# Kernel tuning notes

Hardware: AMD Instinct MI355X
Metric: run time of the kernel (lower is better)

The kernel has to match this reference:

```python
import jax, jax.numpy as jnp
import numpy as np

N_NODES = 50000
N_EDGES = 800000
IN_CH, OUT_CH, HEADS = 64, 32, 4
NEG_SLOPE = 0.2
BN_EPS = 1e-5


def setup_inputs() -> dict:
    key = jax.random.key(0)
    ks = jax.random.split(key, 9)
    x = jax.random.normal(ks[0], (N_NODES, IN_CH), dtype=jnp.float32)
    pos = jax.random.uniform(ks[1], (N_NODES, 3), dtype=jnp.float32)
    edge_index = jax.random.randint(ks[2], (2, N_EDGES), 0, N_NODES, dtype=jnp.int64)
    s = 1.0 / np.sqrt(IN_CH)
    W_l = jax.random.normal(ks[3], (IN_CH, HEADS * OUT_CH), dtype=jnp.float32) * s
    W_r = jax.random.normal(ks[4], (IN_CH, HEADS * OUT_CH), dtype=jnp.float32) * s
    W_edge = jax.random.normal(ks[5], (3, HEADS * OUT_CH), dtype=jnp.float32) * 0.5
    att = jax.random.normal(ks[6], (HEADS, OUT_CH), dtype=jnp.float32) * (1.0 / np.sqrt(OUT_CH))
    bn_gamma = jax.random.uniform(ks[7], (HEADS * OUT_CH,), dtype=jnp.float32, minval=0.5, maxval=1.5)
    bn_beta = jax.random.normal(ks[8], (HEADS * OUT_CH,), dtype=jnp.float32) * 0.1
    return {"x": x, "pos": pos, "edge_index": edge_index, "W_l": W_l, "W_r": W_r,
            "W_edge": W_edge, "att": att, "bn_gamma": bn_gamma, "bn_beta": bn_beta}


def reference(x, pos, edge_index, W_l, W_r, W_edge, att, bn_gamma, bn_beta):
    N = x.shape[0]
    H, C = att.shape
    # source->target projections (GATv2: lin_l for source/messages, lin_r for target)
    xl = (x @ W_l).reshape(N, H, C)
    xr = (x @ W_r).reshape(N, H, C)
    src, dst = edge_index[0], edge_index[1]
    edge_attr = pos[src] - pos[dst]  # [E,3] relative position as edge feature
    # add self-loops with fill_value='mean' (PyG default)
    loop = jnp.arange(N)
    src = jnp.concatenate([src, loop])
    dst = jnp.concatenate([dst, loop])
    mean_attr = edge_attr.mean(axis=0, keepdims=True)  # [1,3]
    edge_attr = jnp.concatenate([edge_attr, jnp.broadcast_to(mean_attr, (N, 3))], axis=0)
    # per-edge GATv2 score: att . LeakyReLU(x_l[j] + x_r[i] + W_e e_ij)
    e_feat = (edge_attr @ W_edge).reshape(-1, H, C)
    msg = xl[src]                              # [Et,H,C] (reused for aggregation)
    e = msg + xr[dst] + e_feat
    e = jax.nn.leaky_relu(e, NEG_SLOPE)
    score = jnp.einsum('ehc,hc->eh', e, att)   # [Et,H]
    # segment softmax over destination node
    m = jax.ops.segment_max(score, dst, num_segments=N)
    score = jnp.exp(score - m[dst])
    denom = jax.ops.segment_sum(score, dst, num_segments=N)
    alpha = score / (denom[dst] + 1e-16)       # [Et,H]
    out = jax.ops.segment_sum(alpha[:, :, None] * msg, dst, num_segments=N)
    out = out.reshape(N, H * C)
    # BatchNorm over node dimension (training-mode batch statistics, PyG BatchNorm)
    mu = out.mean(axis=0)
    var = out.var(axis=0)
    return (out - mu) / jnp.sqrt(var + BN_EPS) * bn_gamma + bn_beta
```

## Files before the change

### kernel.cpp

```cpp
#include <hip/hip_runtime.h>
#include <hip/hip_bf16.h>
#include <hip/hip_fp16.h>

#define N_NODES 50000
#define IN_CH 64
#define HC 128
#define CAP 64
#define NEG_SLOPE 0.2f
#define BN_EPS 1e-5f


__global__ __launch_bounds__(256) void k_gemm(const float* __restrict__ x,
                                              const float* __restrict__ Wl,
                                              const float* __restrict__ Wr,
                                              unsigned int* __restrict__ xl_bf,
                                              float* __restrict__ xr_out,
                                              int* __restrict__ deg,
                                              float* __restrict__ mean_sums,
                                              float* __restrict__ bn_sums,
                                              int* __restrict__ flag,
                                              const int* __restrict__ eidx) {
  {
    int gtid = blockIdx.x * 256 + threadIdx.x;
    if (gtid < N_NODES) deg[gtid] = 1;
    if (gtid < 256) bn_sums[gtid] = 0.f;
    if (gtid < 3) mean_sums[gtid] = 0.f;
    if (blockIdx.x == 0 && threadIdx.x < 64) {
      int w = eidx[2 * threadIdx.x + 1];
      unsigned long long nz = __ballot(w != 0);
      if (threadIdx.x == 0) flag[0] = (nz == 0ULL) ? 1 : 0;
    }
  }

  __shared__ float xs[16][IN_CH];
  __shared__ __hip_bfloat162 wsm[IN_CH][128];
  const int t = threadIdx.x;
  const int row0 = blockIdx.x * 16;

  for (int i = 0; i < 32; ++i) {
    int k = i * 2 + (t >> 7);
    int p = t & 127;
    int cc = p * 2;
    float2 wv;
    if (cc < 128) wv = *(const float2*)(Wl + k * 128 + cc);
    else          wv = *(const float2*)(Wr + k * 128 + (cc - 128));
    wsm[k][p] = __float22bfloat162_rn(wv);
  }
  {
    int r = t >> 4, c4 = (t & 15) * 4;
    *(float4*)&xs[r][c4] = *(const float4*)(x + (row0 + r) * IN_CH + c4);
  }
  __syncthreads();

  const int ct = t & 63;
  const int rt = t >> 6;
  const int c4 = ct * 4;
  const int r4 = rt * 4;

  float acc[4][4];
  #pragma unroll
  for (int a = 0; a < 4; ++a)
    #pragma unroll
    for (int b = 0; b < 4; ++b) acc[a][b] = 0.f;

  #pragma unroll 8
  for (int k = 0; k < IN_CH; ++k) {
    uint2 wraw = *(const uint2*)&wsm[k][ct * 2];
    float2 f01 = __bfloat1622float2(*(__hip_bfloat162*)&wraw.x);
    float2 f23 = __bfloat1622float2(*(__hip_bfloat162*)&wraw.y);
    float wv[4] = {f01.x, f01.y, f23.x, f23.y};
    float xv[4] = {xs[r4][k], xs[r4 + 1][k], xs[r4 + 2][k], xs[r4 + 3][k]};
    #pragma unroll
    for (int a = 0; a < 4; ++a)
      #pragma unroll
      for (int b = 0; b < 4; ++b) acc[a][b] = fmaf(xv[a], wv[b], acc[a][b]);
  }

  #pragma unroll
  for (int a = 0; a < 4; ++a) {
    int row = row0 + r4 + a;
    if (c4 < 128) {
      __hip_bfloat162 b01 = __float22bfloat162_rn(make_float2(acc[a][0], acc[a][1]));
      __hip_bfloat162 b23 = __float22bfloat162_rn(make_float2(acc[a][2], acc[a][3]));
      uint2 u;
      u.x = *(unsigned int*)&b01;
      u.y = *(unsigned int*)&b23;
      *(uint2*)(xl_bf + row * 64 + (c4 >> 1)) = u;
    } else {
      float4 v = make_float4(acc[a][0], acc[a][1], acc[a][2], acc[a][3]);
      *(float4*)(xr_out + row * HC + (c4 - 128)) = v;
    }
  }
}

__device__ __forceinline__ uint2 packslot(int s, float dx, float dy, float dz) {
  __half2 hxy = __halves2half2(__float2half_rn(dx), __float2half_rn(dy));
  uint2 r;
  r.x = *(unsigned int*)&hxy;
  r.y = ((unsigned int)s << 16) | (unsigned int)__half_as_ushort(__float2half_rn(dz));
  return r;
}

__global__ __launch_bounds__(256) void k_edges(const int* __restrict__ eidx,
                                               const float* __restrict__ pos,
                                               int* __restrict__ deg,
                                               uint2* __restrict__ bucket,
                                               float* __restrict__ mean_sums,
                                               const int* __restrict__ flag,
                                               int E) {
  const bool w64 = flag[0] != 0;
  const int tid = blockIdx.x * 256 + threadIdx.x;
  const int base = tid * 8;
  float sx = 0.f, sy = 0.f, sz = 0.f;

  const bool vec_ok = w64 ? ((E & 1) == 0) : ((E & 3) == 0);

  if (base + 8 <= E && vec_ok) {
    int s[8], d[8];
    if (w64) {
      const int4* ps = (const int4*)(eidx + 2 * base);
      int4 A = ps[0], B = ps[1], C = ps[2], D = ps[3];
      s[0]=A.x; s[1]=A.z; s[2]=B.x; s[3]=B.z; s[4]=C.x; s[5]=C.z; s[6]=D.x; s[7]=D.z;
      const int4* pd = (const int4*)(eidx + 2 * E + 2 * base);
      A = pd[0]; B = pd[1]; C = pd[2]; D = pd[3];
      d[0]=A.x; d[1]=A.z; d[2]=B.x; d[3]=B.z; d[4]=C.x; d[5]=C.z; d[6]=D.x; d[7]=D.z;
    } else {
      int4 A = *(const int4*)(eidx + base);
      int4 B = *(const int4*)(eidx + base + 4);
      s[0]=A.x; s[1]=A.y; s[2]=A.z; s[3]=A.w; s[4]=B.x; s[5]=B.y; s[6]=B.z; s[7]=B.w;
      A = *(const int4*)(eidx + E + base);
      B = *(const int4*)(eidx + E + base + 4);
      d[0]=A.x; d[1]=A.y; d[2]=A.z; d[3]=A.w; d[4]=B.x; d[5]=B.y; d[6]=B.z; d[7]=B.w;
    }
    int slot[8];
    #pragma unroll
    for (int k = 0; k < 8; ++k) slot[k] = atomicAdd(&deg[d[k]], 1);
    float dx[8], dy[8], dz[8];
    #pragma unroll
    for (int k = 0; k < 8; ++k) {
      dx[k] = pos[3 * s[k]]     - pos[3 * d[k]];
      dy[k] = pos[3 * s[k] + 1] - pos[3 * d[k] + 1];
      dz[k] = pos[3 * s[k] + 2] - pos[3 * d[k] + 2];
      sx += dx[k]; sy += dy[k]; sz += dz[k];
    }
    #pragma unroll
    for (int k = 0; k < 8; ++k)
      if (slot[k] < CAP) bucket[d[k] * CAP + slot[k]] = packslot(s[k], dx[k], dy[k], dz[k]);
  } else if (base < E) {
    int hi = min(base + 8, E);
    for (int e = base; e < hi; ++e) {
      int s, d;
      if (w64) { s = eidx[2 * e]; d = eidx[2 * (E + e)]; }
      else     { s = eidx[e];     d = eidx[E + e]; }
      int o = atomicAdd(&deg[d], 1);
      float dx = pos[3 * s]     - pos[3 * d];
      float dy = pos[3 * s + 1] - pos[3 * d + 1];
      float dz = pos[3 * s + 2] - pos[3 * d + 2];
      sx += dx; sy += dy; sz += dz;
      if (o < CAP) bucket[d * CAP + o] = packslot(s, dx, dy, dz);
    }
  }

  #pragma unroll
  for (int m = 1; m < 64; m <<= 1) {
    sx += __shfl_xor(sx, m); sy += __shfl_xor(sy, m); sz += __shfl_xor(sz, m);
  }
  __shared__ float red[4][3];
  int wave = threadIdx.x >> 6, lane = threadIdx.x & 63;
  if (lane == 0) { red[wave][0] = sx; red[wave][1] = sy; red[wave][2] = sz; }
  __syncthreads();
  if (threadIdx.x == 0) {
    float a = 0.f, b = 0.f, c = 0.f;
    for (int w = 0; w < 4; ++w) { a += red[w][0]; b += red[w][1]; c += red[w][2]; }
    unsafeAtomicAdd(&mean_sums[0], a);
    unsafeAtomicAdd(&mean_sums[1], b);
    unsafeAtomicAdd(&mean_sums[2], c);
  }
}

__device__ __forceinline__ float sum8_dpp(float v) {
  v += __int_as_float(__builtin_amdgcn_mov_dpp(__float_as_int(v), 0xB1, 0xF, 0xF, true));
  v += __int_as_float(__builtin_amdgcn_mov_dpp(__float_as_int(v), 0x4E, 0xF, 0xF, true));
  v += __int_as_float(__builtin_amdgcn_mov_dpp(__float_as_int(v), 0x141, 0xF, 0xF, true));
  return v;
}

__device__ __forceinline__ void edge_compute(uint2 raw, float dx, float dy, float dz, bool valid,
                                             const float4& xr4, const float4& at4,
                                             const float4& w0, const float4& w1, const float4& w2,
                                             float& a0, float& a1, float& a2, float& a3, float& den) {
  float2 x01 = __bfloat1622float2(*(__hip_bfloat162*)&raw.x);
  float2 x23 = __bfloat1622float2(*(__hip_bfloat162*)&raw.y);
  float t0 = x01.x + xr4.x; t0 = fmaf(dx, w0.x, t0); t0 = fmaf(dy, w1.x, t0); t0 = fmaf(dz, w2.x, t0);
  float t1 = x01.y + xr4.y; t1 = fmaf(dx, w0.y, t1); t1 = fmaf(dy, w1.y, t1); t1 = fmaf(dz, w2.y, t1);
  float t2 = x23.x + xr4.z; t2 = fmaf(dx, w0.z, t2); t2 = fmaf(dy, w1.z, t2); t2 = fmaf(dz, w2.z, t2);
  float t3 = x23.y + xr4.w; t3 = fmaf(dx, w0.w, t3); t3 = fmaf(dy, w1.w, t3); t3 = fmaf(dz, w2.w, t3);
  float l0 = fmaxf(t0, NEG_SLOPE * t0);
  float l1 = fmaxf(t1, NEG_SLOPE * t1);
  float l2 = fmaxf(t2, NEG_SLOPE * t2);
  float l3 = fmaxf(t3, NEG_SLOPE * t3);
  float sc = l0 * at4.x;
  sc = fmaf(l1, at4.y, sc); sc = fmaf(l2, at4.z, sc); sc = fmaf(l3, at4.w, sc);
  sc = sum8_dpp(sc);
  float e = __expf(sc);
  float p = valid ? e : 0.f;
  den += p;
  a0 = fmaf(p, x01.x, a0); a1 = fmaf(p, x01.y, a1);
  a2 = fmaf(p, x23.x, a2); a3 = fmaf(p, x23.y, a3);
}

__device__ __forceinline__ void slotNZ(const uint2* __restrict__ row, int j, int di, int i,
                                       int& s, float& dx, float& dy, float& dz, bool& v) {
  uint2 w = row[j];
  v = j < di;
  s = v ? (int)(w.y >> 16) : i;
  float2 dd = __half22float2(*(__half2*)&w.x);
  dx = dd.x; dy = dd.y;
  dz = __half2float(__ushort_as_half((unsigned short)(w.y & 0xffffu)));
}

__global__ __launch_bounds__(256) void k_agg(const unsigned int* __restrict__ xl_bf,
                                             float* __restrict__ xr_out,
                                             const float* __restrict__ att,
                                             const float* __restrict__ We,
                                             const float* __restrict__ mean_sums,
                                             const uint2* __restrict__ bucket,
                                             const int* __restrict__ deg,
                                             float invE,
                                             float* __restrict__ bn_sums) {
  __shared__ uint2 rowbuf[4][2][72];
  __shared__ __align__(16) float redS[4][128];
  __shared__ __align__(16) float redQ[4][128];

  const int lane = threadIdx.x & 63;
  const int half = lane >> 5;
  const int l5 = lane & 31;
  const int c = l5 << 2;
  const int wave = threadIdx.x >> 6;

  const float4 at4 = *(const float4*)(att + c);
  const float4 w0 = *(const float4*)(We + c);
  const float4 w1 = *(const float4*)(We + 128 + c);
  const float4 w2 = *(const float4*)(We + 256 + c);
  const float m0 = mean_sums[0] * invE;
  const float m1 = mean_sums[1] * invE;
  const float m2 = mean_sums[2] * invE;

  const int gw = blockIdx.x * 4 + wave;
  const int W = gridDim.x * 4;

  float4 bs = make_float4(0.f, 0.f, 0.f, 0.f);
  float4 bq = make_float4(0.f, 0.f, 0.f, 0.f);

  int dcur = min(deg[gw], CAP);
  if (lane < dcur) rowbuf[wave][0][lane] = bucket[gw * CAP + lane];
  int r = 0;

  for (int i = gw; i < N_NODES; i += W) {
    const int inext = i + W;
    int dnext = 0;
    uint2 sregN = make_uint2(0u, 0u);
    if (inext < N_NODES) {
      dnext = min(deg[inext], CAP);
      if (lane < dnext) sregN = bucket[inext * CAP + lane];
    }

    const uint2* row = rowbuf[wave][r];
    const float4 xr4 = *(const float4*)(xr_out + i * HC + c);
    const int di = dcur;

    int sA, sB;
    float dxA, dyA, dzA, dxB, dyB, dzB;
    bool vA, vB;
    if (half == 0) { sA = i; dxA = m0; dyA = m1; dzA = m2; vA = true; }
    else           { slotNZ(row, 1, di, i, sA, dxA, dyA, dzA, vA); }
    slotNZ(row, 2 + half, di, i, sB, dxB, dyB, dzB, vB);
    uint2 rawA = *(const uint2*)(xl_bf + (sA << 6) + (l5 << 1));
    uint2 rawB = *(const uint2*)(xl_bf + (sB << 6) + (l5 << 1));

    float a0 = 0.f, a1 = 0.f, a2 = 0.f, a3 = 0.f, den = 0.f;

    for (int j = 4; j < di; j += 4) {
      int sAn, sBn;
      float dxAn, dyAn, dzAn, dxBn, dyBn, dzBn;
      bool vAn, vBn;
      slotNZ(row, j + half,     di, i, sAn, dxAn, dyAn, dzAn, vAn);
      slotNZ(row, j + 2 + half, di, i, sBn, dxBn, dyBn, dzBn, vBn);
      uint2 rawAn = *(const uint2*)(xl_bf + (sAn << 6) + (l5 << 1));
      uint2 rawBn = *(const uint2*)(xl_bf + (sBn << 6) + (l5 << 1));

      edge_compute(rawA, dxA, dyA, dzA, vA, xr4, at4, w0, w1, w2, a0, a1, a2, a3, den);
      edge_compute(rawB, dxB, dyB, dzB, vB, xr4, at4, w0, w1, w2, a0, a1, a2, a3, den);

      rawA = rawAn; dxA = dxAn; dyA = dyAn; dzA = dzAn; vA = vAn;
      rawB = rawBn; dxB = dxBn; dyB = dyBn; dzB = dzBn; vB = vBn;
    }
    edge_compute(rawA, dxA, dyA, dzA, vA, xr4, at4, w0, w1, w2, a0, a1, a2, a3, den);
    edge_compute(rawB, dxB, dyB, dzB, vB, xr4, at4, w0, w1, w2, a0, a1, a2, a3, den);

    if (lane < dnext) rowbuf[wave][r ^ 1][lane] = sregN;

    den += __shfl_xor(den, 32);
    a0 += __shfl_xor(a0, 32);
    a1 += __shfl_xor(a1, 32);
    a2 += __shfl_xor(a2, 32);
    a3 += __shfl_xor(a3, 32);

    const float inv = 1.f / (den + 1e-16f);
    if (half == 0) {
      float4 o = make_float4(a0 * inv, a1 * inv, a2 * inv, a3 * inv);
      *(float4*)(xr_out + i * HC + c) = o;
      bs.x += o.x; bs.y += o.y; bs.z += o.z; bs.w += o.w;
      bq.x = fmaf(o.x, o.x, bq.x); bq.y = fmaf(o.y, o.y, bq.y);
      bq.z = fmaf(o.z, o.z, bq.z); bq.w = fmaf(o.w, o.w, bq.w);
    }

    dcur = dnext; r ^= 1;
  }

  if (half == 0) {
    *(float4*)&redS[wave][c] = bs;
    *(float4*)&redQ[wave][c] = bq;
  }
  __syncthreads();
  const int t = threadIdx.x;
  if (t < 128) {
    float s = redS[0][t] + redS[1][t] + redS[2][t] + redS[3][t];
    float q = redQ[0][t] + redQ[1][t] + redQ[2][t] + redQ[3][t];
    unsafeAtomicAdd(&bn_sums[t], s);
    unsafeAtomicAdd(&bn_sums[128 + t], q);
  }
}

__global__ __launch_bounds__(256) void k_bnapply(float* __restrict__ out,
                                                 const float* __restrict__ bn_sums,
                                                 const float* __restrict__ gamma,
                                                 const float* __restrict__ beta,
                                                 int n4) {
  const int stride = gridDim.x * blockDim.x;
  const float invN = 1.f / (float)N_NODES;
  for (int i = blockIdx.x * blockDim.x + threadIdx.x; i < n4; i += stride) {
    int c = (i & 31) * 4;
    float4 v = ((float4*)out)[i];
    float4 s = *(const float4*)(bn_sums + c);
    float4 q = *(const float4*)(bn_sums + 128 + c);
    float4 g = *(const float4*)(gamma + c);
    float4 b = *(const float4*)(beta + c);
    float mu, var, rstd;
    mu = s.x * invN; var = q.x * invN - mu * mu; rstd = rsqrtf(var + BN_EPS);
    v.x = (v.x - mu) * rstd * g.x + b.x;
    mu = s.y * invN; var = q.y * invN - mu * mu; rstd = rsqrtf(var + BN_EPS);
    v.y = (v.y - mu) * rstd * g.y + b.y;
    mu = s.z * invN; var = q.z * invN - mu * mu; rstd = rsqrtf(var + BN_EPS);
    v.z = (v.z - mu) * rstd * g.z + b.z;
    mu = s.w * invN; var = q.w * invN - mu * mu; rstd = rsqrtf(var + BN_EPS);
    v.w = (v.w - mu) * rstd * g.w + b.w;
    ((float4*)out)[i] = v;
  }
}

extern "C" void kernel_launch(void* const* d_in, const int* in_sizes, int n_in,
                              void* d_out, int out_size, void* d_ws, size_t ws_size,
                              hipStream_t stream) {
  const float* x     = (const float*)d_in[0];
  const float* pos   = (const float*)d_in[1];
  const int*   eidx  = (const int*)d_in[2];
  const float* Wl    = (const float*)d_in[3];
  const float* Wr    = (const float*)d_in[4];
  const float* We    = (const float*)d_in[5];
  const float* att   = (const float*)d_in[6];
  const float* gamma = (const float*)d_in[7];
  const float* beta  = (const float*)d_in[8];
  float* out = (float*)d_out;
  const int E = in_sizes[2] / 2;

  char* ws = (char*)d_ws;
  int*   flag      = (int*)(ws + 0);
  float* mean_sums = (float*)(ws + 64);
  float* bn_sums   = (float*)(ws + 1024);
  int*   deg       = (int*)(ws + 4096);
  uint2* bucket    = (uint2*)(ws + (1 << 19));
  unsigned int* xl_bf = (unsigned int*)(ws + (1 << 19) + (size_t)N_NODES * CAP * 8);

  k_gemm<<<N_NODES / 16, 256, 0, stream>>>(x, Wl, Wr, xl_bf, out,
                                           deg, mean_sums, bn_sums, flag, eidx);
  int eblocks = (E + 2047) / 2048;
  k_edges<<<eblocks, 256, 0, stream>>>(eidx, pos, deg, bucket, mean_sums, flag, E);
  k_agg<<<2048, 256, 0, stream>>>(xl_bf, out, att, We, mean_sums, bucket, deg,
                                  1.f / (float)E, bn_sums);
  k_bnapply<<<512, 256, 0, stream>>>(out, bn_sums, gamma, beta, out_size / 4);
}
```

Baseline: 243.9 us.

## Process one edge per wave with 2 channels per lane and readlane metadata

The aggregation kernel changes its work split. Each wave now handles one edge at a time, with every lane owning two channels, instead of two half-waves each handling alternate edges with four channels per lane. Edge metadata now sits in registers and is broadcast with readlane, replacing the LDS row buffer. The next node's xr row and self-loop xl row are prefetched as well. This removes LDS traffic, the cross-half shuffles and the padded invalid-slot work, but it serializes edges within a wave and adds one more DPP reduction step per edge.

```diff
diff --git a/kernel.cpp b/kernel.cpp
--- a/kernel.cpp
+++ b/kernel.cpp
@@ -178,45 +178,32 @@
   }
 }
 
-__device__ __forceinline__ float sum8_dpp(float v) {
-  v += __int_as_float(__builtin_amdgcn_mov_dpp(__float_as_int(v), 0xB1, 0xF, 0xF, true));
-  v += __int_as_float(__builtin_amdgcn_mov_dpp(__float_as_int(v), 0x4E, 0xF, 0xF, true));
+__device__ __forceinline__ float sum16_dpp(float v) {
+  v += __int_as_float(__builtin_amdgcn_mov_dpp(__float_as_int(v), 0xB1,  0xF, 0xF, true));
+  v += __int_as_float(__builtin_amdgcn_mov_dpp(__float_as_int(v), 0x4E,  0xF, 0xF, true));
   v += __int_as_float(__builtin_amdgcn_mov_dpp(__float_as_int(v), 0x141, 0xF, 0xF, true));
+  v += __int_as_float(__builtin_amdgcn_mov_dpp(__float_as_int(v), 0x140, 0xF, 0xF, true));
   return v;
 }
 
-__device__ __forceinline__ void edge_compute(uint2 raw, float dx, float dy, float dz, bool valid,
-                                             const float4& xr4, const float4& at4,
-                                             const float4& w0, const float4& w1, const float4& w2,
-                                             float& a0, float& a1, float& a2, float& a3, float& den) {
-  float2 x01 = __bfloat1622float2(*(__hip_bfloat162*)&raw.x);
-  float2 x23 = __bfloat1622float2(*(__hip_bfloat162*)&raw.y);
-  float t0 = x01.x + xr4.x; t0 = fmaf(dx, w0.x, t0); t0 = fmaf(dy, w1.x, t0); t0 = fmaf(dz, w2.x, t0);
-  float t1 = x01.y + xr4.y; t1 = fmaf(dx, w0.y, t1); t1 = fmaf(dy, w1.y, t1); t1 = fmaf(dz, w2.y, t1);
-  float t2 = x23.x + xr4.z; t2 = fmaf(dx, w0.z, t2); t2 = fmaf(dy, w1.z, t2); t2 = fmaf(dz, w2.z, t2);
-  float t3 = x23.y + xr4.w; t3 = fmaf(dx, w0.w, t3); t3 = fmaf(dy, w1.w, t3); t3 = fmaf(dz, w2.w, t3);
+__device__ __forceinline__ void edge2(unsigned raw, float dx, float dy, float dz,
+                                      const float2& xr2, const float2& at2,
+                                      const float2& w0, const float2& w1, const float2& w2,
+                                      float& den, float& a0, float& a1) {
+  float x0 = __uint_as_float(raw << 16);
+  float x1 = __uint_as_float(raw & 0xffff0000u);
+  float t0 = x0 + xr2.x;
+  t0 = fmaf(dx, w0.x, t0); t0 = fmaf(dy, w1.x, t0); t0 = fmaf(dz, w2.x, t0);
+  float t1 = x1 + xr2.y;
+  t1 = fmaf(dx, w0.y, t1); t1 = fmaf(dy, w1.y, t1); t1 = fmaf(dz, w2.y, t1);
   float l0 = fmaxf(t0, NEG_SLOPE * t0);
   float l1 = fmaxf(t1, NEG_SLOPE * t1);
-  float l2 = fmaxf(t2, NEG_SLOPE * t2);
-  float l3 = fmaxf(t3, NEG_SLOPE * t3);
-  float sc = l0 * at4.x;
-  sc = fmaf(l1, at4.y, sc); sc = fmaf(l2, at4.z, sc); sc = fmaf(l3, at4.w, sc);
-  sc = sum8_dpp(sc);
-  float e = __expf(sc);
-  float p = valid ? e : 0.f;
+  float sc = l0 * at2.x;
+  sc = fmaf(l1, at2.y, sc);
+  sc = sum16_dpp(sc);
+  float p = __expf(sc);
   den += p;
-  a0 = fmaf(p, x01.x, a0); a1 = fmaf(p, x01.y, a1);
-  a2 = fmaf(p, x23.x, a2); a3 = fmaf(p, x23.y, a3);
-}
-
-__device__ __forceinline__ void slotNZ(const uint2* __restrict__ row, int j, int di, int i,
-                                       int& s, float& dx, float& dy, float& dz, bool& v) {
-  uint2 w = row[j];
-  v = j < di;
-  s = v ? (int)(w.y >> 16) : i;
-  float2 dd = __half22float2(*(__half2*)&w.x);
-  dx = dd.x; dy = dd.y;
-  dz = __half2float(__ushort_as_half((unsigned short)(w.y & 0xffffu)));
+  a0 = fmaf(p, x0, a0); a1 = fmaf(p, x1, a1);
 }
 
 __global__ __launch_bounds__(256) void k_agg(const unsigned int* __restrict__ xl_bf,
@@ -228,20 +215,17 @@
                                              const int* __restrict__ deg,
                                              float invE,
                                              float* __restrict__ bn_sums) {
-  __shared__ uint2 rowbuf[4][2][72];
   __shared__ __align__(16) float redS[4][128];
   __shared__ __align__(16) float redQ[4][128];
 
   const int lane = threadIdx.x & 63;
-  const int half = lane >> 5;
-  const int l5 = lane & 31;
-  const int c = l5 << 2;
   const int wave = threadIdx.x >> 6;
-
-  const float4 at4 = *(const float4*)(att + c);
-  const float4 w0 = *(const float4*)(We + c);
-  const float4 w1 = *(const float4*)(We + 128 + c);
-  const float4 w2 = *(const float4*)(We + 256 + c);
+  const int c2 = lane << 1;
+
+  const float2 at2 = *(const float2*)(att + c2);
+  const float2 w0 = *(const float2*)(We + c2);
+  const float2 w1 = *(const float2*)(We + 128 + c2);
+  const float2 w2 = *(const float2*)(We + 256 + c2);
   const float m0 = mean_sums[0] * invE;
   const float m1 = mean_sums[1] * invE;
   const float m2 = mean_sums[2] * invE;
@@ -249,79 +233,72 @@
   const int gw = blockIdx.x * 4 + wave;
   const int W = gridDim.x * 4;
 
-  float4 bs = make_float4(0.f, 0.f, 0.f, 0.f);
-  float4 bq = make_float4(0.f, 0.f, 0.f, 0.f);
-
-  int dcur = min(deg[gw], CAP);
-  if (lane < dcur) rowbuf[wave][0][lane] = bucket[gw * CAP + lane];
-  int r = 0;
+  float bsx = 0.f, bsy = 0.f, bqx = 0.f, bqy = 0.f;
+
+  int dcur = 0;
+  uint2 rowc = make_uint2(0u, 0u);
+  float2 xrc = make_float2(0.f, 0.f);
+  unsigned xlsc = 0u;
+  if (gw < N_NODES) {
+    dcur = min(deg[gw], CAP);
+    rowc = bucket[(size_t)gw * CAP + lane];
+    xrc = *(const float2*)(xr_out + gw * HC + c2);
+    xlsc = xl_bf[gw * 64 + lane];
+  }
 
   for (int i = gw; i < N_NODES; i += W) {
     const int inext = i + W;
     int dnext = 0;
-    uint2 sregN = make_uint2(0u, 0u);
+    uint2 rown = make_uint2(0u, 0u);
+    float2 xrn = make_float2(0.f, 0.f);
+    unsigned xlsn = 0u;
     if (inext < N_NODES) {
       dnext = min(deg[inext], CAP);
-      if (lane < dnext) sregN = bucket[inext * CAP + lane];
-    }
-
-    const uint2* row = rowbuf[wave][r];
-    const float4 xr4 = *(const float4*)(xr_out + i * HC + c);
+      rown = bucket[(size_t)inext * CAP + lane];
+      xrn = *(const float2*)(xr_out + inext * HC + c2);
+      xlsn = xl_bf[inext * 64 + lane];
+    }
+
     const int di = dcur;
-
-    int sA, sB;
-    float dxA, dyA, dzA, dxB, dyB, dzB;
-    bool vA, vB;
-    if (half == 0) { sA = i; dxA = m0; dyA = m1; dzA = m2; vA = true; }
-    else           { slotNZ(row, 1, di, i, sA, dxA, dyA, dzA, vA); }
-    slotNZ(row, 2 + half, di, i, sB, dxB, dyB, dzB, vB);
-    uint2 rawA = *(const uint2*)(xl_bf + (sA << 6) + (l5 << 1));
-    uint2 rawB = *(const uint2*)(xl_bf + (sB << 6) + (l5 << 1));
-
-    float a0 = 0.f, a1 = 0.f, a2 = 0.f, a3 = 0.f, den = 0.f;
-
-    for (int j = 4; j < di; j += 4) {
-      int sAn, sBn;
-      float dxAn, dyAn, dzAn, dxBn, dyBn, dzBn;
-      bool vAn, vBn;
-      slotNZ(row, j + half,     di, i, sAn, dxAn, dyAn, dzAn, vAn);
-      slotNZ(row, j + 2 + half, di, i, sBn, dxBn, dyBn, dzBn, vBn);
-      uint2 rawAn = *(const uint2*)(xl_bf + (sAn << 6) + (l5 << 1));
-      uint2 rawBn = *(const uint2*)(xl_bf + (sBn << 6) + (l5 << 1));
-
-      edge_compute(rawA, dxA, dyA, dzA, vA, xr4, at4, w0, w1, w2, a0, a1, a2, a3, den);
-      edge_compute(rawB, dxB, dyB, dzB, vB, xr4, at4, w0, w1, w2, a0, a1, a2, a3, den);
-
-      rawA = rawAn; dxA = dxAn; dyA = dyAn; dzA = dzAn; vA = vAn;
-      rawB = rawBn; dxB = dxBn; dyB = dyBn; dzB = dzBn; vB = vBn;
-    }
-    edge_compute(rawA, dxA, dyA, dzA, vA, xr4, at4, w0, w1, w2, a0, a1, a2, a3, den);
-    edge_compute(rawB, dxB, dyB, dzB, vB, xr4, at4, w0, w1, w2, a0, a1, a2, a3, den);
-
-    if (lane < dnext) rowbuf[wave][r ^ 1][lane] = sregN;
-
-    den += __shfl_xor(den, 32);
-    a0 += __shfl_xor(a0, 32);
-    a1 += __shfl_xor(a1, 32);
-    a2 += __shfl_xor(a2, 32);
-    a3 += __shfl_xor(a3, 32);
+    float den = 0.f, a0 = 0.f, a1 = 0.f;
+
+    edge2(xlsc, m0, m1, m2, xrc, at2, w0, w1, w2, den, a0, a1);
+
+    if (di > 1) {
+      int wx = __builtin_amdgcn_readlane((int)rowc.x, 1);
+      int wy = __builtin_amdgcn_readlane((int)rowc.y, 1);
+      unsigned raw = xl_bf[((unsigned)wy >> 16) * 64u + (unsigned)lane];
+      for (int j = 1;;) {
+        const int jn = j + 1;
+        const bool more = jn < di;
+        int wxn = 0, wyn = 0;
+        unsigned rawn = 0u;
+        if (more) {
+          wxn = __builtin_amdgcn_readlane((int)rowc.x, jn);
+          wyn = __builtin_amdgcn_readlane((int)rowc.y, jn);
+          rawn = xl_bf[((unsigned)wyn >> 16) * 64u + (unsigned)lane];
+        }
+        float dx = __half2float(__ushort_as_half((unsigned short)(wx & 0xffff)));
+        float dy = __half2float(__ushort_as_half((unsigned short)((unsigned)wx >> 16)));
+        float dz = __half2float(__ushort_as_half((unsigned short)(wy & 0xffff)));
+        edge2(raw, dx, dy, dz, xrc, at2, w0, w1, w2, den, a0, a1);
+        if (!more) break;
+        wx = wxn; wy = wyn; raw = rawn; j = jn;
+      }
+    }
 
     const float inv = 1.f / (den + 1e-16f);
-    if (half == 0) {
-      float4 o = make_float4(a0 * inv, a1 * inv, a2 * inv, a3 * inv);
-      *(float4*)(xr_out + i * HC + c) = o;
-      bs.x += o.x; bs.y += o.y; bs.z += o.z; bs.w += o.w;
-      bq.x = fmaf(o.x, o.x, bq.x); bq.y = fmaf(o.y, o.y, bq.y);
-      bq.z = fmaf(o.z, o.z, bq.z); bq.w = fmaf(o.w, o.w, bq.w);
-    }
-
-    dcur = dnext; r ^= 1;
-  }
-
-  if (half == 0) {
-    *(float4*)&redS[wave][c] = bs;
-    *(float4*)&redQ[wave][c] = bq;
-  }
+    const float o0 = a0 * inv;
+    const float o1 = a1 * inv;
+    *(float2*)(xr_out + i * HC + c2) = make_float2(o0, o1);
+    bsx += o0; bsy += o1;
+    bqx = fmaf(o0, o0, bqx); bqy = fmaf(o1, o1, bqy);
+
+    dcur = dnext; rowc = rown; xrc = xrn; xlsc = xlsn;
+  }
+
+  *(float2*)&redS[wave][c2] = make_float2(bsx, bsy);
+  *(float2*)&redQ[wave][c2] = make_float2(bqx, bqy);
   __syncthreads();
   const int t = threadIdx.x;
   if (t < 128) {
```

After: 271.8 us. +11.4%, slower.
